# Kernel optimization log

Hardware: AMD Instinct MI355X
Metric: run time of the kernel (lower is better)

## Reference

```python
import jax, jax.numpy as jnp
import numpy as np

B, S, E, H = 2, 2048, 2048, 16
HD = E // H  # head_dim = 128


def setup_inputs() -> dict:
    key = jax.random.key(0)
    ks = jax.random.split(key, 7)
    inp = {
        "query": jax.random.normal(ks[0], (B, S, E), dtype=jnp.float32),
        "key": jax.random.normal(ks[1], (B, S, E), dtype=jnp.float32),
        "value": jax.random.normal(ks[2], (B, S, E), dtype=jnp.float32),
        # qkv: Linear(E, 3E) -> weight [3E, E], bias [3E]
        "Wqkv": jax.random.normal(ks[3], (3 * E, E), dtype=jnp.float32) * (E ** -0.5),
        "bqkv": jnp.zeros((3 * E,), dtype=jnp.float32),
        # proj: Linear(E, E) (source bug-fixed; see notes)
        "Wproj": jax.random.normal(ks[4], (E, E), dtype=jnp.float32) * (E ** -0.5),
        "bproj": jnp.zeros((E,), dtype=jnp.float32),
    }
    return inp


def reference(query, key, value, Wqkv, bqkv, Wproj, bproj):
    # NB: `key` and `value` are unused by the original forward.
    b, s, _ = query.shape
    qkv = query @ Wqkv.T + bqkv                      # [B, S, 3E]
    qkv = qkv.reshape(b, s, H, 3 * HD).transpose(0, 2, 1, 3)  # [B, H, S, 3*HD]
    q = qkv[..., :HD]
    k = qkv[..., HD:2 * HD]
    v = qkv[..., 2 * HD:]
    # Source divides by scale_factor = HD**-0.5, i.e. MULTIPLIES by sqrt(HD).
    scores = jnp.einsum("bhqd,bhkd->bhqk", q, k) * (HD ** 0.5)
    attn = jax.nn.softmax(scores, axis=-1)           # dropout p=0 -> identity
    out = jnp.einsum("bhqk,bhkd->bhqd", attn, v)     # [B, H, S, HD]
    out = out.transpose(0, 2, 1, 3).reshape(b, s, E)  # [B, S, E]
    return out @ Wproj.T + bproj
```

## Files before the change

### kernel.cpp

```cpp
#include <hip/hip_runtime.h>

#define B_  2
#define S_  2048
#define E_  2048
#define H_  16
#define HD_ 128
#define M_  (B_*S_)
#define N1_ (3*E_)
#define K_  E_

typedef _Float16 f16;
typedef __attribute__((ext_vector_type(8))) _Float16 f16x8;
typedef __attribute__((ext_vector_type(4))) _Float16 f16x4;
typedef __attribute__((ext_vector_type(4))) float    f32x4;
typedef __attribute__((ext_vector_type(4))) float    fv4;

__device__ __forceinline__ void async16(const f16* g, f16* l) {
    __builtin_amdgcn_global_load_lds(
        (const __attribute__((address_space(1))) unsigned int*)g,
        (__attribute__((address_space(3))) unsigned int*)l, 16, 0, 0);
}

__device__ __forceinline__ int swz8(int row, int g) {
    return row * 64 + ((g ^ (row & 7)) << 3);
}
__device__ __forceinline__ int swz16(int row, int g) {
    return row * 128 + ((g ^ (row & 15)) << 3);
}

__device__ __forceinline__ void stage_swz8(const f16* __restrict__ src, int ldg,
                                           f16* lds, int w, int lane) {
#pragma unroll
    for (int i = 0; i < 4; ++i) {
        int p = (w * 4 + i) * 64 + lane;
        int row = p >> 3, gl = p & 7;
        int gs = gl ^ (row & 7);
        async16(src + (size_t)row * ldg + gs * 8, lds + (size_t)p * 8);
    }
}

__device__ __forceinline__ void stage_k64(const f16* __restrict__ src, f16* lds, int t) {
#pragma unroll
    for (int i = 0; i < 4; ++i) {
        int p = i * 256 + t;
        int row = p >> 4, gl = p & 15;
        int gs = gl ^ (row & 15);
        async16(src + (size_t)row * 128 + gs * 8, lds + (size_t)p * 8);
    }
}
__device__ __forceinline__ void stage_v64(const f16* __restrict__ src, f16* lds, int t) {
#pragma unroll
    for (int i = 0; i < 4; ++i) {
        int p = i * 256 + t;
        int row = p >> 3, gl = p & 7;
        int gs = gl ^ (row & 7);
        async16(src + (size_t)row * 2048 + gs * 8, lds + (size_t)p * 8);
    }
}

__device__ __forceinline__ void split8(fv4 a0, fv4 a1, float scale, f16x8& hi, f16x8& lo) {
    float x[8] = {a0.x, a0.y, a0.z, a0.w, a1.x, a1.y, a1.z, a1.w};
#pragma unroll
    for (int e = 0; e < 8; ++e) {
        float xs = x[e] * scale;
        f16 h = (f16)xs;
        hi[e] = h;
        lo[e] = (f16)(xs - (float)h);
    }
}

__global__ void split_f32(const float* __restrict__ src, f16* __restrict__ hi,
                          f16* __restrict__ lo, float scale, int n8) {
    int i = blockIdx.x * blockDim.x + threadIdx.x;
    if (i < n8) {
        fv4 a0 = ((const fv4*)src)[2 * i];
        fv4 a1 = ((const fv4*)src)[2 * i + 1];
        f16x8 h, l;
        split8(a0, a1, scale, h, l);
        ((f16x8*)hi)[i] = h;
        ((f16x8*)lo)[i] = l;
    }
}

__global__ void cvt_f32_f16(const float* __restrict__ src, f16* __restrict__ dst, int n4) {
    int i = blockIdx.x * blockDim.x + threadIdx.x;
    if (i < n4) {
        fv4 v = ((const fv4*)src)[i];
        f16x4 h;
        h.x = (f16)v.x; h.y = (f16)v.y; h.z = (f16)v.z; h.w = (f16)v.w;
        ((f16x4*)dst)[i] = h;
    }
}

template <bool AsyncA>
__global__ __launch_bounds__(256) void gemm_qkv(
    const float* __restrict__ A, const f16* __restrict__ A_hi, const f16* __restrict__ A_lo,
    const f16* __restrict__ W_hi, const f16* __restrict__ W_lo, const float* __restrict__ bias,
    f16* __restrict__ qh, f16* __restrict__ kh, f16* __restrict__ vT)
{
    __shared__ f16 As_hi[128 * 64];
    __shared__ f16 As_lo[128 * 64];
    __shared__ f16 Bs_hi[128 * 64];
    __shared__ f16 Bs_lo[128 * 64];
    const int t = threadIdx.x;
    const int w = t >> 6, lane = t & 63, quad = lane >> 4, l15 = lane & 15;
    const int m0 = blockIdx.y * 128, n0 = blockIdx.x * 128;
    const int wm = (w & 1) * 64, wn = (w >> 1) * 64;
    const int tile_part = (n0 % 384) >> 7;
    const bool need_lo = (tile_part != 2);

    f32x4 acc[4][4];
#pragma unroll
    for (int i = 0; i < 4; ++i)
#pragma unroll
        for (int j = 0; j < 4; ++j) { acc[i][j].x = 0.f; acc[i][j].y = 0.f; acc[i][j].z = 0.f; acc[i][j].w = 0.f; }

    for (int kb = 0; kb < K_ / 64; ++kb) {
        stage_swz8(W_hi + (size_t)n0 * K_ + kb * 64, K_, Bs_hi, w, lane);
        if (need_lo)
            stage_swz8(W_lo + (size_t)n0 * K_ + kb * 64, K_, Bs_lo, w, lane);
        if (AsyncA) {
            stage_swz8(A_hi + (size_t)m0 * K_ + kb * 64, K_, As_hi, w, lane);
            if (need_lo)
                stage_swz8(A_lo + (size_t)m0 * K_ + kb * 64, K_, As_lo, w, lane);
        } else {
            const float* Ag = A + (size_t)m0 * K_ + kb * 64;
#pragma unroll
            for (int i = 0; i < 4; ++i) {
                int gid = t + i * 256;
                int row = gid >> 3, g = gid & 7;
                const float* ap = Ag + (size_t)row * K_ + g * 8;
                fv4 a0 = *(const fv4*)ap;
                fv4 a1 = *(const fv4*)(ap + 4);
                f16x8 hi, lo;
                split8(a0, a1, 1.0f, hi, lo);
                *(f16x8*)&As_hi[swz8(row, g)] = hi;
                *(f16x8*)&As_lo[swz8(row, g)] = lo;
            }
        }
        __syncthreads();

#pragma unroll
        for (int ks = 0; ks < 2; ++ks) {
            f16x8 ah[4], al[4], bh[4], bl[4];
            int g = ks * 4 + quad;
#pragma unroll
            for (int mt = 0; mt < 4; ++mt) {
                int row = wm + mt * 16 + l15;
                ah[mt] = *(const f16x8*)&As_hi[swz8(row, g)];
                al[mt] = *(const f16x8*)&As_lo[swz8(row, g)];
            }
#pragma unroll
            for (int nt = 0; nt < 4; ++nt) {
                int row = wn + nt * 16 + l15;
                bh[nt] = *(const f16x8*)&Bs_hi[swz8(row, g)];
                bl[nt] = *(const f16x8*)&Bs_lo[swz8(row, g)];
            }
#pragma unroll
            for (int mt = 0; mt < 4; ++mt)
#pragma unroll
                for (int nt = 0; nt < 4; ++nt) {
                    acc[mt][nt] = __builtin_amdgcn_mfma_f32_16x16x32_f16(ah[mt], bh[nt], acc[mt][nt], 0, 0, 0);
                    if (need_lo) {
                        acc[mt][nt] = __builtin_amdgcn_mfma_f32_16x16x32_f16(ah[mt], bl[nt], acc[mt][nt], 0, 0, 0);
                        acc[mt][nt] = __builtin_amdgcn_mfma_f32_16x16x32_f16(al[mt], bh[nt], acc[mt][nt], 0, 0, 0);
                    }
                }
        }
        __syncthreads();
    }

    const float inv_s = 1.0f / 64.0f;
#pragma unroll
    for (int nt = 0; nt < 4; ++nt) {
        int n = n0 + wn + nt * 16 + l15;
        float bs = bias[n];
        int h = n / 384;
        int r = n % 384;
        int part = r >> 7;
        int d = r & 127;
#pragma unroll
        for (int mt = 0; mt < 4; ++mt) {
            int mbase = m0 + wm + mt * 16 + quad * 4;
            int b = mbase >> 11, s = mbase & 2047;
            int bh = b * H_ + h;
            if (part == 2) {
                f16x4 pv;
                pv.x = (f16)(acc[mt][nt].x * inv_s + bs);
                pv.y = (f16)(acc[mt][nt].y * inv_s + bs);
                pv.z = (f16)(acc[mt][nt].z * inv_s + bs);
                pv.w = (f16)(acc[mt][nt].w * inv_s + bs);
                *(f16x4*)&vT[((size_t)bh * 128 + d) * 2048 + s] = pv;
            } else {
                f16* dst = (part == 0) ? qh : kh;
                size_t base = (size_t)bh * 2048 * 128;
#pragma unroll
                for (int reg = 0; reg < 4; ++reg)
                    dst[base + (size_t)(s + reg) * 128 + d] = (f16)(acc[mt][nt][reg] * inv_s + bs);
            }
        }
    }
}

__global__ __launch_bounds__(256) void attn(
    const f16* __restrict__ qh, const f16* __restrict__ kh, const f16* __restrict__ vT,
    f16* __restrict__ ao)
{
    __shared__ f16 Kb[2][64 * 128];
    __shared__ f16 Vb[2][128 * 64];
    __shared__ f16 Ps[128 * 64];
    const int t = threadIdx.x;
    const int w = t >> 6, lane = t & 63, quad = lane >> 4, l15 = lane & 15;
    const int bh = blockIdx.y;
    const int q0 = blockIdx.x * 128;
    const f16* Q  = qh + (size_t)bh * 2048 * 128;
    const f16* Kp = kh + (size_t)bh * 2048 * 128;
    const f16* Vp = vT + (size_t)bh * 128 * 2048;

    const float C2 = (float)(11.313708498984761 * 1.4426950408889634);

    f16x8 qf[2][4];
#pragma unroll
    for (int mt = 0; mt < 2; ++mt)
#pragma unroll
        for (int ks = 0; ks < 4; ++ks) {
            int row = q0 + w * 32 + mt * 16 + l15;
            qf[mt][ks] = *(const f16x8*)&Q[(size_t)row * 128 + ks * 32 + quad * 8];
        }

    f32x4 o[2][8];
    float mrow[2][4], lrow[2][4];
#pragma unroll
    for (int mt = 0; mt < 2; ++mt) {
#pragma unroll
        for (int dt = 0; dt < 8; ++dt) { o[mt][dt].x = 0.f; o[mt][dt].y = 0.f; o[mt][dt].z = 0.f; o[mt][dt].w = 0.f; }
#pragma unroll
        for (int reg = 0; reg < 4; ++reg) { mrow[mt][reg] = -1e30f; lrow[mt][reg] = 0.f; }
    }

    stage_k64(Kp, Kb[0], t);
    stage_v64(Vp, Vb[0], t);

    for (int j = 0; j < 32; ++j) {
        __syncthreads();
        const int cur = j & 1;
        if (j < 31) {
            stage_k64(Kp + (size_t)(j + 1) * 64 * 128, Kb[cur ^ 1], t);
            stage_v64(Vp + (j + 1) * 64, Vb[cur ^ 1], t);
        }

        f32x4 sa[2][4];
#pragma unroll
        for (int mt = 0; mt < 2; ++mt)
#pragma unroll
            for (int nt = 0; nt < 4; ++nt) { sa[mt][nt].x = 0.f; sa[mt][nt].y = 0.f; sa[mt][nt].z = 0.f; sa[mt][nt].w = 0.f; }
#pragma unroll
        for (int ks = 0; ks < 4; ++ks) {
            int g = ks * 4 + quad;
            f16x8 bf[4];
#pragma unroll
            for (int nt = 0; nt < 4; ++nt) { int row = nt * 16 + l15; bf[nt] = *(const f16x8*)&Kb[cur][swz16(row, g)]; }
#pragma unroll
            for (int mt = 0; mt < 2; ++mt)
#pragma unroll
                for (int nt = 0; nt < 4; ++nt)
                    sa[mt][nt] = __builtin_amdgcn_mfma_f32_16x16x32_f16(qf[mt][ks], bf[nt], sa[mt][nt], 0, 0, 0);
        }

        float mnew[2][4], alpha[2][4];
#pragma unroll
        for (int mt = 0; mt < 2; ++mt)
#pragma unroll
            for (int reg = 0; reg < 4; ++reg) {
                float mx = sa[mt][0][reg];
#pragma unroll
                for (int nt = 1; nt < 4; ++nt) mx = fmaxf(mx, sa[mt][nt][reg]);
                mx *= C2;
#pragma unroll
                for (int d = 1; d < 16; d <<= 1) mx = fmaxf(mx, __shfl_xor(mx, d));
                float mn = fmaxf(mrow[mt][reg], mx);
                mnew[mt][reg]  = mn;
                alpha[mt][reg] = exp2f(mrow[mt][reg] - mn);
                mrow[mt][reg]  = mn;
            }
#pragma unroll
        for (int mt = 0; mt < 2; ++mt)
#pragma unroll
            for (int reg = 0; reg < 4; ++reg) {
                float rs = 0.f;
#pragma unroll
                for (int nt = 0; nt < 4; ++nt) {
                    float p = exp2f(sa[mt][nt][reg] * C2 - mnew[mt][reg]);
                    sa[mt][nt][reg] = p;
                    rs += p;
                }
#pragma unroll
                for (int d = 1; d < 16; d <<= 1) rs += __shfl_xor(rs, d);
                lrow[mt][reg] = lrow[mt][reg] * alpha[mt][reg] + rs;
#pragma unroll
                for (int dt = 0; dt < 8; ++dt) o[mt][dt][reg] *= alpha[mt][reg];
            }

#pragma unroll
        for (int mt = 0; mt < 2; ++mt)
#pragma unroll
            for (int nt = 0; nt < 4; ++nt) {
                int col = nt * 16 + l15;
#pragma unroll
                for (int reg = 0; reg < 4; ++reg) {
                    int row = w * 32 + mt * 16 + quad * 4 + reg;
                    Ps[row * 64 + (((col >> 3) ^ (row & 7)) << 3) + (col & 7)] = (f16)sa[mt][nt][reg];
                }
            }

#pragma unroll
        for (int ks = 0; ks < 2; ++ks) {
            int g = ks * 4 + quad;
            f16x8 pf[2], vf[8];
#pragma unroll
            for (int mt = 0; mt < 2; ++mt) { int row = w * 32 + mt * 16 + l15; pf[mt] = *(const f16x8*)&Ps[swz8(row, g)]; }
#pragma unroll
            for (int dt = 0; dt < 8; ++dt) { int row = dt * 16 + l15; vf[dt] = *(const f16x8*)&Vb[cur][swz8(row, g)]; }
#pragma unroll
            for (int mt = 0; mt < 2; ++mt)
#pragma unroll
                for (int dt = 0; dt < 8; ++dt)
                    o[mt][dt] = __builtin_amdgcn_mfma_f32_16x16x32_f16(pf[mt], vf[dt], o[mt][dt], 0, 0, 0);
        }
    }

    const int b = bh >> 4, h = bh & 15;
#pragma unroll
    for (int mt = 0; mt < 2; ++mt) {
        float inv[4];
#pragma unroll
        for (int reg = 0; reg < 4; ++reg) inv[reg] = 1.0f / lrow[mt][reg];
#pragma unroll
        for (int dt = 0; dt < 8; ++dt) {
            int col = h * 128 + dt * 16 + l15;
#pragma unroll
            for (int reg = 0; reg < 4; ++reg) {
                int srow = q0 + w * 32 + mt * 16 + quad * 4 + reg;
                ao[(size_t)((b << 11) + srow) * 2048 + col] = (f16)(o[mt][dt][reg] * inv[reg]);
            }
        }
    }
}

__global__ __launch_bounds__(256) void gemm_proj(
    const f16* __restrict__ A, const f16* __restrict__ W, const float* __restrict__ bias,
    float* __restrict__ out)
{
    __shared__ f16 As[128 * 64];
    __shared__ f16 Bs[128 * 64];
    const int t = threadIdx.x;
    const int w = t >> 6, lane = t & 63, quad = lane >> 4, l15 = lane & 15;
    const int m0 = blockIdx.y * 128, n0 = blockIdx.x * 128;
    const int wm = (w & 1) * 64, wn = (w >> 1) * 64;

    f32x4 acc[4][4];
#pragma unroll
    for (int i = 0; i < 4; ++i)
#pragma unroll
        for (int j = 0; j < 4; ++j) { acc[i][j].x = 0.f; acc[i][j].y = 0.f; acc[i][j].z = 0.f; acc[i][j].w = 0.f; }

    for (int kb = 0; kb < K_ / 64; ++kb) {
        stage_swz8(A + (size_t)m0 * K_ + kb * 64, K_, As, w, lane);
        stage_swz8(W + (size_t)n0 * K_ + kb * 64, K_, Bs, w, lane);
        __syncthreads();
#pragma unroll
        for (int ks = 0; ks < 2; ++ks) {
            f16x8 af[4], bf[4];
            int g = ks * 4 + quad;
#pragma unroll
            for (int mt = 0; mt < 4; ++mt) { int row = wm + mt * 16 + l15; af[mt] = *(const f16x8*)&As[swz8(row, g)]; }
#pragma unroll
            for (int nt = 0; nt < 4; ++nt) { int row = wn + nt * 16 + l15; bf[nt] = *(const f16x8*)&Bs[swz8(row, g)]; }
#pragma unroll
            for (int mt = 0; mt < 4; ++mt)
#pragma unroll
                for (int nt = 0; nt < 4; ++nt)
                    acc[mt][nt] = __builtin_amdgcn_mfma_f32_16x16x32_f16(af[mt], bf[nt], acc[mt][nt], 0, 0, 0);
        }
        __syncthreads();
    }

#pragma unroll
    for (int nt = 0; nt < 4; ++nt) {
        int n = n0 + wn + nt * 16 + l15;
        float bs = bias[n];
#pragma unroll
        for (int mt = 0; mt < 4; ++mt) {
            int mbase = m0 + wm + mt * 16 + quad * 4;
#pragma unroll
            for (int reg = 0; reg < 4; ++reg)
                out[(size_t)(mbase + reg) * 2048 + n] = acc[mt][nt][reg] + bs;
        }
    }
}

extern "C" void kernel_launch(void* const* d_in, const int* in_sizes, int n_in,
                              void* d_out, int out_size, void* d_ws, size_t ws_size,
                              hipStream_t stream) {
    const float* query = (const float*)d_in[0];
    const float* Wqkv  = (const float*)d_in[3];
    const float* bqkv  = (const float*)d_in[4];
    const float* Wproj = (const float*)d_in[5];
    const float* bproj = (const float*)d_in[6];
    float* out = (float*)d_out;

    char* ws = (char*)d_ws;
    const size_t MB = 1024ull * 1024ull;
    const bool big = (ws_size >= 128 * MB);

    f16 *A_hi, *A_lo, *W_hi, *W_lo, *qh, *kh, *vT, *ao, *w2;
    if (big) {
        A_hi = (f16*)(ws);
        A_lo = (f16*)(ws + 16 * MB);
        W_hi = (f16*)(ws + 32 * MB);
        W_lo = (f16*)(ws + 56 * MB);
        qh   = (f16*)(ws + 80 * MB);
        kh   = (f16*)(ws + 96 * MB);
        vT   = (f16*)(ws + 112 * MB);
        ao   = (f16*)(ws);
        w2   = (f16*)(ws + 56 * MB);
    } else {
        if (ws_size < 96 * MB) return;
        A_hi = A_lo = nullptr;
        W_hi = (f16*)(ws);
        W_lo = (f16*)(ws + 24 * MB);
        qh   = (f16*)(ws + 48 * MB);
        kh   = (f16*)(ws + 64 * MB);
        vT   = (f16*)(ws + 80 * MB);
        ao   = (f16*)(ws);
        w2   = (f16*)(ws + 24 * MB);
    }

    if (big)
        split_f32<<<(M_ * K_ / 8 + 255) / 256, 256, 0, stream>>>(query, A_hi, A_lo, 1.0f, M_ * K_ / 8);
    split_f32<<<(N1_ * K_ / 8 + 255) / 256, 256, 0, stream>>>(Wqkv, W_hi, W_lo, 64.0f, N1_ * K_ / 8);

    if (big)
        gemm_qkv<true><<<dim3(N1_ / 128, M_ / 128), 256, 0, stream>>>(query, A_hi, A_lo, W_hi, W_lo, bqkv, qh, kh, vT);
    else
        gemm_qkv<false><<<dim3(N1_ / 128, M_ / 128), 256, 0, stream>>>(query, A_hi, A_lo, W_hi, W_lo, bqkv, qh, kh, vT);

    cvt_f32_f16<<<(E_ * E_ / 4 + 255) / 256, 256, 0, stream>>>(Wproj, w2, E_ * E_ / 4);

    attn<<<dim3(S_ / 128, B_ * H_), 256, 0, stream>>>(qh, kh, vT, ao);
    gemm_proj<<<dim3(E_ / 128, M_ / 128), 256, 0, stream>>>(ao, w2, bproj, out);
}
```

Baseline: 707.1 us.

## Single-buffer K/V in attention, defer row-sum reduction, skip unchanged rescales

The attention kernel drops double-buffered K/V staging in favour of a single LDS buffer, loaded each iteration between two barriers. The per-row softmax sum is now kept as a per-lane partial and reduced across lanes once at the end rather than every tile. The output and sum rescale is skipped when no row maximum in the wavefront grew. Less LDS may allow higher occupancy and fewer shuffles per tile, but loads are no longer overlapped with compute and a data-dependent branch is added.

```diff
diff --git a/kernel.cpp b/kernel.cpp
--- a/kernel.cpp
+++ b/kernel.cpp
@@ -206,8 +206,8 @@
     const f16* __restrict__ qh, const f16* __restrict__ kh, const f16* __restrict__ vT,
     f16* __restrict__ ao)
 {
-    __shared__ f16 Kb[2][64 * 128];
-    __shared__ f16 Vb[2][128 * 64];
+    __shared__ f16 Ks[64 * 128];
+    __shared__ f16 Vts[128 * 64];
     __shared__ f16 Ps[128 * 64];
     const int t = threadIdx.x;
     const int w = t >> 6, lane = t & 63, quad = lane >> 4, l15 = lane & 15;
@@ -229,25 +229,20 @@
         }
 
     f32x4 o[2][8];
-    float mrow[2][4], lrow[2][4];
+    float mrow[2][4], lpart[2][4];
 #pragma unroll
     for (int mt = 0; mt < 2; ++mt) {
 #pragma unroll
         for (int dt = 0; dt < 8; ++dt) { o[mt][dt].x = 0.f; o[mt][dt].y = 0.f; o[mt][dt].z = 0.f; o[mt][dt].w = 0.f; }
 #pragma unroll
-        for (int reg = 0; reg < 4; ++reg) { mrow[mt][reg] = -1e30f; lrow[mt][reg] = 0.f; }
-    }
-
-    stage_k64(Kp, Kb[0], t);
-    stage_v64(Vp, Vb[0], t);
+        for (int reg = 0; reg < 4; ++reg) { mrow[mt][reg] = -1e30f; lpart[mt][reg] = 0.f; }
+    }
 
     for (int j = 0; j < 32; ++j) {
         __syncthreads();
-        const int cur = j & 1;
-        if (j < 31) {
-            stage_k64(Kp + (size_t)(j + 1) * 64 * 128, Kb[cur ^ 1], t);
-            stage_v64(Vp + (j + 1) * 64, Vb[cur ^ 1], t);
-        }
+        stage_k64(Kp + (size_t)j * 64 * 128, Ks, t);
+        stage_v64(Vp + j * 64, Vts, t);
+        __syncthreads();
 
         f32x4 sa[2][4];
 #pragma unroll
@@ -259,7 +254,7 @@
             int g = ks * 4 + quad;
             f16x8 bf[4];
 #pragma unroll
-            for (int nt = 0; nt < 4; ++nt) { int row = nt * 16 + l15; bf[nt] = *(const f16x8*)&Kb[cur][swz16(row, g)]; }
+            for (int nt = 0; nt < 4; ++nt) { int row = nt * 16 + l15; bf[nt] = *(const f16x8*)&Ks[swz16(row, g)]; }
 #pragma unroll
             for (int mt = 0; mt < 2; ++mt)
 #pragma unroll
@@ -267,7 +262,8 @@
                     sa[mt][nt] = __builtin_amdgcn_mfma_f32_16x16x32_f16(qf[mt][ks], bf[nt], sa[mt][nt], 0, 0, 0);
         }
 
-        float mnew[2][4], alpha[2][4];
+        float mnew[2][4];
+        bool changed = false;
 #pragma unroll
         for (int mt = 0; mt < 2; ++mt)
 #pragma unroll
@@ -278,11 +274,21 @@
                 mx *= C2;
 #pragma unroll
                 for (int d = 1; d < 16; d <<= 1) mx = fmaxf(mx, __shfl_xor(mx, d));
-                float mn = fmaxf(mrow[mt][reg], mx);
-                mnew[mt][reg]  = mn;
-                alpha[mt][reg] = exp2f(mrow[mt][reg] - mn);
-                mrow[mt][reg]  = mn;
-            }
+                if (mx > mrow[mt][reg]) changed = true;
+                mnew[mt][reg] = fmaxf(mrow[mt][reg], mx);
+            }
+        if (__any(changed)) {
+#pragma unroll
+            for (int mt = 0; mt < 2; ++mt)
+#pragma unroll
+                for (int reg = 0; reg < 4; ++reg) {
+                    float alpha = exp2f(mrow[mt][reg] - mnew[mt][reg]);
+                    mrow[mt][reg] = mnew[mt][reg];
+                    lpart[mt][reg] *= alpha;
+#pragma unroll
+                    for (int dt = 0; dt < 8; ++dt) o[mt][dt][reg] *= alpha;
+                }
+        }
 #pragma unroll
         for (int mt = 0; mt < 2; ++mt)
 #pragma unroll
@@ -290,15 +296,11 @@
                 float rs = 0.f;
 #pragma unroll
                 for (int nt = 0; nt < 4; ++nt) {
-                    float p = exp2f(sa[mt][nt][reg] * C2 - mnew[mt][reg]);
+                    float p = exp2f(sa[mt][nt][reg] * C2 - mrow[mt][reg]);
                     sa[mt][nt][reg] = p;
                     rs += p;
                 }
-#pragma unroll
-                for (int d = 1; d < 16; d <<= 1) rs += __shfl_xor(rs, d);
-                lrow[mt][reg] = lrow[mt][reg] * alpha[mt][reg] + rs;
-#pragma unroll
-                for (int dt = 0; dt < 8; ++dt) o[mt][dt][reg] *= alpha[mt][reg];
+                lpart[mt][reg] += rs;
             }
 
 #pragma unroll
@@ -320,7 +322,7 @@
 #pragma unroll
             for (int mt = 0; mt < 2; ++mt) { int row = w * 32 + mt * 16 + l15; pf[mt] = *(const f16x8*)&Ps[swz8(row, g)]; }
 #pragma unroll
-            for (int dt = 0; dt < 8; ++dt) { int row = dt * 16 + l15; vf[dt] = *(const f16x8*)&Vb[cur][swz8(row, g)]; }
+            for (int dt = 0; dt < 8; ++dt) { int row = dt * 16 + l15; vf[dt] = *(const f16x8*)&Vts[swz8(row, g)]; }
 #pragma unroll
             for (int mt = 0; mt < 2; ++mt)
 #pragma unroll
@@ -329,12 +331,20 @@
         }
     }
 
+#pragma unroll
+    for (int mt = 0; mt < 2; ++mt)
+#pragma unroll
+        for (int reg = 0; reg < 4; ++reg) {
+#pragma unroll
+            for (int d = 1; d < 16; d <<= 1) lpart[mt][reg] += __shfl_xor(lpart[mt][reg], d);
+        }
+
     const int b = bh >> 4, h = bh & 15;
 #pragma unroll
     for (int mt = 0; mt < 2; ++mt) {
         float inv[4];
 #pragma unroll
-        for (int reg = 0; reg < 4; ++reg) inv[reg] = 1.0f / lrow[mt][reg];
+        for (int reg = 0; reg < 4; ++reg) inv[reg] = 1.0f / lpart[mt][reg];
 #pragma unroll
         for (int dt = 0; dt < 8; ++dt) {
             int col = h * 128 + dt * 16 + l15;
```

Result: faster. 640.8 us (-9.4%).
